# Optimization experiments

Measured on AMD Instinct MI355X. Metric: run time of the kernel, lower is better.

Reference implementation:

```python
import jax, jax.numpy as jnp
import numpy as np

N = 65536      # points
C = 256        # channels
K = 16         # knn_samples
L = 4          # num_blocks
EXP = 4        # MLP expansion
EPS = 1e-5


def layer_norm(x, g, b):
    m = jnp.mean(x, axis=-1, keepdims=True)
    v = jnp.var(x, axis=-1, keepdims=True)
    return (x - m) * jax.lax.rsqrt(v + EPS) * g + b


def setup_inputs() -> dict:
    key = jax.random.key(0)
    ks = jax.random.split(key, 16)
    s = lambda fan_in: 1.0 / np.sqrt(fan_in)
    inp = {
        "x": jax.random.normal(ks[0], (N, C), jnp.float32),
        "knn_idx": jax.random.randint(ks[1], (N, K), 0, N, jnp.int32),
        # per-block stacked params (PyTorch Linear stored as [in, out] here)
        "ln1_g": jnp.ones((L, C), jnp.float32),
        "ln1_b": jnp.zeros((L, C), jnp.float32),
        "w_qkv": jax.random.uniform(ks[2], (L, C, 3 * C), jnp.float32, -s(C), s(C)),
        "w_proj": jax.random.uniform(ks[3], (L, C, C), jnp.float32, -s(C), s(C)),
        "b_proj": jax.random.uniform(ks[4], (L, C), jnp.float32, -s(C), s(C)),
        "ln2_g": jnp.ones((L, C), jnp.float32),
        "ln2_b": jnp.zeros((L, C), jnp.float32),
        "w_fc1": jax.random.uniform(ks[5], (L, C, EXP * C), jnp.float32, -s(C), s(C)),
        "b_fc1": jax.random.uniform(ks[6], (L, EXP * C), jnp.float32, -s(C), s(C)),
        "w_fc2": jax.random.uniform(ks[7], (L, EXP * C, C), jnp.float32, -s(EXP * C), s(EXP * C)),
        "b_fc2": jax.random.uniform(ks[8], (L, C), jnp.float32, -s(EXP * C), s(EXP * C)),
    }
    return inp


def reference(x, knn_idx, ln1_g, ln1_b, w_qkv, w_proj, b_proj,
              ln2_g, ln2_b, w_fc1, b_fc1, w_fc2, b_fc2):
    scale = C ** (-0.5)  # head_dim == C (num_heads == 1)
    for i in range(L):
        # --- KNN attention ---
        h = layer_norm(x, ln1_g[i], ln1_b[i])
        qkv = h @ w_qkv[i]                       # [N, 3C], no bias
        q, k, v = jnp.split(qkv, 3, axis=-1)     # each [N, C]
        kk = k[knn_idx]                          # [N, K, C] neighbor gather
        vv = v[knn_idx]                          # [N, K, C]
        scores = jnp.einsum('nc,nkc->nk', q, kk) * scale
        attn = jax.nn.softmax(scores, axis=-1)   # softmax over K neighbors
        out = jnp.einsum('nk,nkc->nc', attn, vv)
        x = x + (out @ w_proj[i] + b_proj[i])
        # --- MLP ---
        h2 = layer_norm(x, ln2_g[i], ln2_b[i])
        h2 = jax.nn.gelu(h2 @ w_fc1[i] + b_fc1[i], approximate=False)
        x = x + (h2 @ w_fc2[i] + b_fc2[i])
    return x
```

## Files before the change

### kernel.cpp

```cpp
#include <hip/hip_runtime.h>

typedef __attribute__((ext_vector_type(4))) float  f32x4;
typedef __attribute__((ext_vector_type(2))) float  f32x2;
typedef __attribute__((ext_vector_type(8))) __bf16 bf16x8;
typedef __attribute__((ext_vector_type(4))) short  s16x4;
typedef __attribute__((ext_vector_type(8))) short  s16x8;
typedef unsigned char uchar;

__device__ __forceinline__ unsigned short f2bf(float f) {
  unsigned u = __builtin_bit_cast(unsigned, f);
  u += 0x7FFFu + ((u >> 16) & 1u);
  return (unsigned short)(u >> 16);
}
__device__ __forceinline__ float b2f(short s) {
  return __builtin_bit_cast(float, (unsigned)((unsigned short)s) << 16);
}
__device__ __forceinline__ uchar f2fp8(float v) {
  return (uchar)(__builtin_amdgcn_cvt_pk_fp8_f32(v, v, 0, false) & 0xFF);
}

__device__ __forceinline__ void gload16(const void* g, void* l) {
  __builtin_amdgcn_global_load_lds(
      (const __attribute__((address_space(1))) void*)g,
      (__attribute__((address_space(3))) void*)l, 16, 0, 0);
}

__global__ __launch_bounds__(256) void wcast(const float* __restrict__ W,
                                             short* __restrict__ WT,
                                             int In, int Out) {
  int i = blockIdx.x * 256 + threadIdx.x;
  int lay = blockIdx.y;
  if (i >= In * Out) return;
  const float* w = W + (size_t)lay * In * Out;
  short* wt = WT + (size_t)lay * In * Out;
  int ii = i % In, oo = i / In;
  wt[(size_t)oo * In + ii] = (short)f2bf(w[(size_t)ii * Out + oo]);
}

__global__ __launch_bounds__(256) void ln_k(const float* __restrict__ x,
                                            const float* __restrict__ g,
                                            const float* __restrict__ b,
                                            short* __restrict__ out) {
  int row = blockIdx.x * 4 + (threadIdx.x >> 6);
  int l = threadIdx.x & 63;
  const float4 v = *(const float4*)(x + (size_t)row * 256 + l * 4);
  float s  = v.x + v.y + v.z + v.w;
  float ss = v.x * v.x + v.y * v.y + v.z * v.z + v.w * v.w;
#pragma unroll
  for (int o = 32; o >= 1; o >>= 1) {
    s  += __shfl_xor(s, o);
    ss += __shfl_xor(ss, o);
  }
  float mean = s * (1.0f / 256.0f);
  float var  = ss * (1.0f / 256.0f) - mean * mean;
  float rstd = rsqrtf(var + 1e-5f);
  const float4 gg = *(const float4*)(g + l * 4);
  const float4 bb = *(const float4*)(b + l * 4);
  s16x4 o4;
  o4[0] = (short)f2bf((v.x - mean) * rstd * gg.x + bb.x);
  o4[1] = (short)f2bf((v.y - mean) * rstd * gg.y + bb.y);
  o4[2] = (short)f2bf((v.z - mean) * rstd * gg.z + bb.z);
  o4[3] = (short)f2bf((v.w - mean) * rstd * gg.w + bb.w);
  *(s16x4*)(out + (size_t)row * 256 + l * 4) = o4;
}

__global__ __launch_bounds__(256) void attn_k(const short* __restrict__ q_,
                                              const uchar* __restrict__ k8,
                                              const uchar* __restrict__ v8,
                                              const int* __restrict__ knn,
                                              short* __restrict__ out) {
  int n = blockIdx.x * 4 + (threadIdx.x >> 6);
  int l = threadIdx.x & 63;
  int j = l & 15, g = l >> 4;
  int idxj = knn[(size_t)n * 16 + j];
  const short* qp = q_ + (size_t)n * 256 + g * 64;
  const uchar* kp = k8 + (size_t)idxj * 256 + g * 64;
  float partial = 0.f;
#pragma unroll
  for (int t = 0; t < 4; ++t) {
    int4 kv = *(const int4*)(kp + t * 16);
    s16x8 q0 = *(const s16x8*)(qp + t * 16);
    s16x8 q1 = *(const s16x8*)(qp + t * 16 + 8);
    f32x2 a;
    a = __builtin_amdgcn_cvt_pk_f32_fp8(kv.x, false);
    partial += a[0] * b2f(q0[0]) + a[1] * b2f(q0[1]);
    a = __builtin_amdgcn_cvt_pk_f32_fp8(kv.x, true);
    partial += a[0] * b2f(q0[2]) + a[1] * b2f(q0[3]);
    a = __builtin_amdgcn_cvt_pk_f32_fp8(kv.y, false);
    partial += a[0] * b2f(q0[4]) + a[1] * b2f(q0[5]);
    a = __builtin_amdgcn_cvt_pk_f32_fp8(kv.y, true);
    partial += a[0] * b2f(q0[6]) + a[1] * b2f(q0[7]);
    a = __builtin_amdgcn_cvt_pk_f32_fp8(kv.z, false);
    partial += a[0] * b2f(q1[0]) + a[1] * b2f(q1[1]);
    a = __builtin_amdgcn_cvt_pk_f32_fp8(kv.z, true);
    partial += a[0] * b2f(q1[2]) + a[1] * b2f(q1[3]);
    a = __builtin_amdgcn_cvt_pk_f32_fp8(kv.w, false);
    partial += a[0] * b2f(q1[4]) + a[1] * b2f(q1[5]);
    a = __builtin_amdgcn_cvt_pk_f32_fp8(kv.w, true);
    partial += a[0] * b2f(q1[6]) + a[1] * b2f(q1[7]);
  }
  partial += __shfl_xor(partial, 16);
  partial += __shfl_xor(partial, 32);
  float score = partial * 0.0625f;
  float mx = score;
#pragma unroll
  for (int o = 1; o < 16; o <<= 1) mx = fmaxf(mx, __shfl_xor(mx, o));
  float e = __expf(score - mx);
  float sum = e;
#pragma unroll
  for (int o = 1; o < 16; o <<= 1) sum += __shfl_xor(sum, o);
  float attn = e / sum;
  float4 o4 = {0.f, 0.f, 0.f, 0.f};
#pragma unroll
  for (int jj = 0; jj < 16; ++jj) {
    float aj = __shfl(attn, jj);
    int   ij = __shfl(idxj, jj);
    int vv = *(const int*)(v8 + (size_t)ij * 256 + l * 4);
    f32x2 lo = __builtin_amdgcn_cvt_pk_f32_fp8(vv, false);
    f32x2 hi = __builtin_amdgcn_cvt_pk_f32_fp8(vv, true);
    o4.x += aj * lo[0];
    o4.y += aj * lo[1];
    o4.z += aj * hi[0];
    o4.w += aj * hi[1];
  }
  s16x4 ob;
  ob[0] = (short)f2bf(o4.x);
  ob[1] = (short)f2bf(o4.y);
  ob[2] = (short)f2bf(o4.z);
  ob[3] = (short)f2bf(o4.w);
  *(s16x4*)(out + (size_t)n * 256 + l * 4) = ob;
}

template <int EPI, int KD>
__global__ __launch_bounds__(256) void gemm_k(
    const short* __restrict__ A, const short* __restrict__ BT,
    const float* __restrict__ bias, const float* __restrict__ resid,
    short* __restrict__ outb, float* __restrict__ outf,
    uchar* __restrict__ k8, uchar* __restrict__ v8, int Nout, int gx) {
  __shared__ __align__(16) short lA[128 * 64];
  __shared__ __align__(16) short lB[128 * 64];
  const int tid = threadIdx.x;
  const int l = tid & 63, w = tid >> 6;
  const int nwg = gridDim.x;
  const int bid = blockIdx.x;
  const int swz = (bid & 7) * (nwg >> 3) + (bid >> 3);
  const int m0 = (swz / gx) << 7, n0 = (swz % gx) << 7;
  const int wm = w >> 1, wn = w & 1;

  f32x4 acc[4][4];
#pragma unroll
  for (int i = 0; i < 4; ++i)
#pragma unroll
    for (int jj = 0; jj < 4; ++jj) acc[i][jj] = f32x4{0.f, 0.f, 0.f, 0.f};

  const int srow = (w << 3) + (l >> 3);
  const int scol = (((l & 7) << 3)) ^ ((srow & 7) << 3);
  const short* gA = A + (size_t)(m0 + srow) * KD + scol;
  const short* gB = BT + (size_t)(n0 + srow) * KD + scol;

  for (int kt = 0; kt < KD; kt += 64) {
#pragma unroll
    for (int it = 0; it < 4; ++it) {
      gload16(gA + (size_t)(it * 32) * KD + kt, &lA[(it * 32 + w * 8) * 64]);
      gload16(gB + (size_t)(it * 32) * KD + kt, &lB[(it * 32 + w * 8) * 64]);
    }
    __syncthreads();
#pragma unroll
    for (int kc = 0; kc < 2; ++kc) {
      bf16x8 aF[4], bF[4];
#pragma unroll
      for (int f = 0; f < 4; ++f) {
        int r = wm * 64 + f * 16 + (l & 15);
        int ce = (kc * 32 + ((l >> 4) << 3)) ^ ((r & 7) << 3);
        aF[f] = *(const bf16x8*)(lA + r * 64 + ce);
      }
#pragma unroll
      for (int f = 0; f < 4; ++f) {
        int r = wn * 64 + f * 16 + (l & 15);
        int ce = (kc * 32 + ((l >> 4) << 3)) ^ ((r & 7) << 3);
        bF[f] = *(const bf16x8*)(lB + r * 64 + ce);
      }
#pragma unroll
      for (int mf = 0; mf < 4; ++mf)
#pragma unroll
        for (int nf = 0; nf < 4; ++nf)
          acc[mf][nf] = __builtin_amdgcn_mfma_f32_16x16x32_bf16(
              aF[mf], bF[nf], acc[mf][nf], 0, 0, 0);
    }
    __syncthreads();
  }

  const int lr = (l >> 4) << 2, lc = l & 15;
#pragma unroll
  for (int mf = 0; mf < 4; ++mf) {
#pragma unroll
    for (int nf = 0; nf < 4; ++nf) {
#pragma unroll
      for (int jj = 0; jj < 4; ++jj) {
        int row = m0 + wm * 64 + mf * 16 + lr + jj;
        int col = n0 + wn * 64 + nf * 16 + lc;
        float v = acc[mf][nf][jj];
        if (EPI == 1) {
          v += bias[col] + resid[(size_t)row * 256 + col];
          outf[(size_t)row * 256 + col] = v;
        } else if (EPI == 2) {
          v += bias[col];
          v = 0.5f * v * (1.f + erff(v * 0.70710678118654752440f));
          outb[(size_t)row * Nout + col] = (short)f2bf(v);
        } else {
          if (col < 256)
            outb[(size_t)row * 256 + col] = (short)f2bf(v);
          else if (col < 512)
            k8[(size_t)row * 256 + (col - 256)] = f2fp8(v);
          else
            v8[(size_t)row * 256 + (col - 512)] = f2fp8(v);
        }
      }
    }
  }
}

extern "C" void kernel_launch(void* const* d_in, const int* in_sizes, int n_in,
                              void* d_out, int out_size, void* d_ws, size_t ws_size,
                              hipStream_t stream) {
  const float* in_x   = (const float*)d_in[0];
  const int*   knn    = (const int*)d_in[1];
  const float* ln1_g  = (const float*)d_in[2];
  const float* ln1_b  = (const float*)d_in[3];
  const float* w_qkv  = (const float*)d_in[4];
  const float* w_proj = (const float*)d_in[5];
  const float* b_proj = (const float*)d_in[6];
  const float* ln2_g  = (const float*)d_in[7];
  const float* ln2_b  = (const float*)d_in[8];
  const float* w_fc1  = (const float*)d_in[9];
  const float* b_fc1  = (const float*)d_in[10];
  const float* w_fc2  = (const float*)d_in[11];
  const float* b_fc2  = (const float*)d_in[12];

  char* ws = (char*)d_ws;
  float* x   = (float*)(ws);
  short* act = (short*)(ws + 67108864);
  short* big = (short*)(ws + 100663296);
  short* q_bf = big;
  uchar* k8   = (uchar*)(ws + 100663296 + 33554432);
  uchar* v8   = (uchar*)(ws + 100663296 + 50331648);
  short* wT  = (short*)(ws + 234881024);
  short* wqkvT  = wT;
  short* wprojT = wT + 786432;
  short* wfc1T  = wT + 1048576;
  short* wfc2T  = wT + 2097152;

  wcast<<<dim3(768, 4), 256, 0, stream>>>(w_qkv, wqkvT, 256, 768);
  wcast<<<dim3(256, 4), 256, 0, stream>>>(w_proj, wprojT, 256, 256);
  wcast<<<dim3(1024, 4), 256, 0, stream>>>(w_fc1, wfc1T, 256, 1024);
  wcast<<<dim3(1024, 4), 256, 0, stream>>>(w_fc2, wfc2T, 1024, 256);

  for (int i = 0; i < 4; ++i) {
    const float* xin = (i == 0) ? in_x : x;
    ln_k<<<16384, 256, 0, stream>>>(xin, ln1_g + i * 256, ln1_b + i * 256, act);
    gemm_k<3, 256><<<3072, 256, 0, stream>>>(
        act, wqkvT + (size_t)i * 196608, nullptr, nullptr, q_bf, nullptr,
        k8, v8, 768, 6);
    attn_k<<<16384, 256, 0, stream>>>(q_bf, k8, v8, knn, act);
    gemm_k<1, 256><<<1024, 256, 0, stream>>>(
        act, wprojT + (size_t)i * 65536, b_proj + i * 256, xin, nullptr, x,
        nullptr, nullptr, 256, 2);
    ln_k<<<16384, 256, 0, stream>>>(x, ln2_g + i * 256, ln2_b + i * 256, act);
    gemm_k<2, 256><<<4096, 256, 0, stream>>>(
        act, wfc1T + (size_t)i * 262144, b_fc1 + i * 1024, nullptr, big, nullptr,
        nullptr, nullptr, 1024, 8);
    gemm_k<1, 1024><<<1024, 256, 0, stream>>>(
        big, wfc2T + (size_t)i * 262144, b_fc2 + i * 256, x, nullptr,
        (i == 3) ? (float*)d_out : x, nullptr, nullptr, 256, 2);
  }
}
```

Measured before the change: 1.320 ms.

## Fuse LayerNorm into residual GEMM epilogues and use tanh-approx GELU

Adds a gemm_ln kernel that computes a full 128x256 output row tile per workgroup. Its epilogue adds bias and residual, writes x, reduces row mean and variance across waves through LDS, and writes the next LayerNorm's bf16 activations. This removes the separate ln_k launches and their re-read of x, and prefetches LN1 for the next block. It also replaces erf-based GELU with a tanh approximation built on __expf. The wider tile raises register pressure (acc[4][8]), halves the grid to 512 workgroups, and the GELU approximation changes numerics.

```diff
diff --git a/kernel.cpp b/kernel.cpp
--- a/kernel.cpp
+++ b/kernel.cpp
@@ -17,6 +17,13 @@
 }
 __device__ __forceinline__ uchar f2fp8(float v) {
   return (uchar)(__builtin_amdgcn_cvt_pk_fp8_f32(v, v, 0, false) & 0xFF);
+}
+__device__ __forceinline__ float gelu_fast(float v) {
+  float u = v * (0.7978845608f + 0.0356774081f * v * v);
+  float t = __expf(-2.f * fabsf(u));
+  float th = (1.f - t) / (1.f + t);
+  th = (u >= 0.f) ? th : -th;
+  return 0.5f * v * (1.f + th);
 }
 
 __device__ __forceinline__ void gload16(const void* g, void* l) {
@@ -134,8 +141,7 @@
 template <int EPI, int KD>
 __global__ __launch_bounds__(256) void gemm_k(
     const short* __restrict__ A, const short* __restrict__ BT,
-    const float* __restrict__ bias, const float* __restrict__ resid,
-    short* __restrict__ outb, float* __restrict__ outf,
+    const float* __restrict__ bias, short* __restrict__ outb,
     uchar* __restrict__ k8, uchar* __restrict__ v8, int Nout, int gx) {
   __shared__ __align__(16) short lA[128 * 64];
   __shared__ __align__(16) short lB[128 * 64];
@@ -200,12 +206,8 @@
         int row = m0 + wm * 64 + mf * 16 + lr + jj;
         int col = n0 + wn * 64 + nf * 16 + lc;
         float v = acc[mf][nf][jj];
-        if (EPI == 1) {
-          v += bias[col] + resid[(size_t)row * 256 + col];
-          outf[(size_t)row * 256 + col] = v;
-        } else if (EPI == 2) {
-          v += bias[col];
-          v = 0.5f * v * (1.f + erff(v * 0.70710678118654752440f));
+        if (EPI == 2) {
+          v = gelu_fast(v + bias[col]);
           outb[(size_t)row * Nout + col] = (short)f2bf(v);
         } else {
           if (col < 256)
@@ -215,6 +217,117 @@
           else
             v8[(size_t)row * 256 + (col - 512)] = f2fp8(v);
         }
+      }
+    }
+  }
+}
+
+template <int KD>
+__global__ __launch_bounds__(256) void gemm_ln(
+    const short* __restrict__ A, const short* __restrict__ BT,
+    const float* __restrict__ bias, const float* __restrict__ resid,
+    float* __restrict__ xout, const float* __restrict__ lng,
+    const float* __restrict__ lnb, short* __restrict__ act) {
+  __shared__ __align__(16) short lA[128 * 64];
+  __shared__ __align__(16) short lB[256 * 64];
+  __shared__ float psum[2][128], psq[2][128];
+  const int tid = threadIdx.x;
+  const int l = tid & 63, w = tid >> 6;
+  const int nwg = gridDim.x;
+  const int bid = blockIdx.x;
+  const int swz = (bid & 7) * (nwg >> 3) + (bid >> 3);
+  const int m0 = swz << 7;
+  const int wm = w >> 1, wn = w & 1;
+
+  f32x4 acc[4][8];
+#pragma unroll
+  for (int i = 0; i < 4; ++i)
+#pragma unroll
+    for (int jj = 0; jj < 8; ++jj) acc[i][jj] = f32x4{0.f, 0.f, 0.f, 0.f};
+
+  const int srow = (w << 3) + (l >> 3);
+  const int scol = (((l & 7) << 3)) ^ ((srow & 7) << 3);
+  const short* gA = A + (size_t)(m0 + srow) * KD + scol;
+  const short* gB = BT + (size_t)srow * KD + scol;
+
+  for (int kt = 0; kt < KD; kt += 64) {
+#pragma unroll
+    for (int it = 0; it < 4; ++it)
+      gload16(gA + (size_t)(it * 32) * KD + kt, &lA[(it * 32 + w * 8) * 64]);
+#pragma unroll
+    for (int it = 0; it < 8; ++it)
+      gload16(gB + (size_t)(it * 32) * KD + kt, &lB[(it * 32 + w * 8) * 64]);
+    __syncthreads();
+#pragma unroll
+    for (int kc = 0; kc < 2; ++kc) {
+      bf16x8 aF[4], bF[8];
+#pragma unroll
+      for (int f = 0; f < 4; ++f) {
+        int r = wm * 64 + f * 16 + (l & 15);
+        int ce = (kc * 32 + ((l >> 4) << 3)) ^ ((r & 7) << 3);
+        aF[f] = *(const bf16x8*)(lA + r * 64 + ce);
+      }
+#pragma unroll
+      for (int f = 0; f < 8; ++f) {
+        int r = wn * 128 + f * 16 + (l & 15);
+        int ce = (kc * 32 + ((l >> 4) << 3)) ^ ((r & 7) << 3);
+        bF[f] = *(const bf16x8*)(lB + r * 64 + ce);
+      }
+#pragma unroll
+      for (int mf = 0; mf < 4; ++mf)
+#pragma unroll
+        for (int nf = 0; nf < 8; ++nf)
+          acc[mf][nf] = __builtin_amdgcn_mfma_f32_16x16x32_bf16(
+              aF[mf], bF[nf], acc[mf][nf], 0, 0, 0);
+    }
+    __syncthreads();
+  }
+
+  const int lr = (l >> 4) << 2, lc = l & 15;
+#pragma unroll
+  for (int mf = 0; mf < 4; ++mf) {
+#pragma unroll
+    for (int jj = 0; jj < 4; ++jj) {
+      int rowl = wm * 64 + mf * 16 + lr + jj;
+      int row = m0 + rowl;
+      float s = 0.f, q = 0.f;
+#pragma unroll
+      for (int nf = 0; nf < 8; ++nf) {
+        int col = wn * 128 + nf * 16 + lc;
+        float v = acc[mf][nf][jj] + bias[col] + resid[(size_t)row * 256 + col];
+        acc[mf][nf][jj] = v;
+        xout[(size_t)row * 256 + col] = v;
+        s += v;
+        q += v * v;
+      }
+#pragma unroll
+      for (int off = 1; off < 16; off <<= 1) {
+        s += __shfl_xor(s, off);
+        q += __shfl_xor(q, off);
+      }
+      if (lc == 0) {
+        psum[wn][rowl] = s;
+        psq[wn][rowl] = q;
+      }
+    }
+  }
+  __syncthreads();
+#pragma unroll
+  for (int mf = 0; mf < 4; ++mf) {
+#pragma unroll
+    for (int jj = 0; jj < 4; ++jj) {
+      int rowl = wm * 64 + mf * 16 + lr + jj;
+      int row = m0 + rowl;
+      float S = psum[0][rowl] + psum[1][rowl];
+      float Q = psq[0][rowl] + psq[1][rowl];
+      float mean = S * (1.0f / 256.0f);
+      float var = Q * (1.0f / 256.0f) - mean * mean;
+      float rstd = rsqrtf(var + 1e-5f);
+#pragma unroll
+      for (int nf = 0; nf < 8; ++nf) {
+        int col = wn * 128 + nf * 16 + lc;
+        float v = (acc[mf][nf][jj] - mean) * rstd * lng[col] + lnb[col];
+        act[(size_t)row * 256 + col] = (short)f2bf(v);
       }
     }
   }
@@ -238,13 +351,14 @@
   const float* b_fc2  = (const float*)d_in[12];
 
   char* ws = (char*)d_ws;
-  float* x   = (float*)(ws);
-  short* act = (short*)(ws + 67108864);
-  short* big = (short*)(ws + 100663296);
+  float* x    = (float*)(ws);
+  short* act  = (short*)(ws + 67108864);
+  short* big  = (short*)(ws + 100663296);
   short* q_bf = big;
-  uchar* k8   = (uchar*)(ws + 100663296 + 33554432);
-  uchar* v8   = (uchar*)(ws + 100663296 + 50331648);
-  short* wT  = (short*)(ws + 234881024);
+  uchar* k8   = (uchar*)(ws + 134217728);
+  uchar* v8   = (uchar*)(ws + 150994944);
+  short* attb = (short*)(ws + 167772160);
+  short* wT   = (short*)(ws + 234881024);
   short* wqkvT  = wT;
   short* wprojT = wT + 786432;
   short* wfc1T  = wT + 1048576;
@@ -255,22 +369,23 @@
   wcast<<<dim3(1024, 4), 256, 0, stream>>>(w_fc1, wfc1T, 256, 1024);
   wcast<<<dim3(1024, 4), 256, 0, stream>>>(w_fc2, wfc2T, 1024, 256);
 
+  ln_k<<<16384, 256, 0, stream>>>(in_x, ln1_g, ln1_b, act);
+
   for (int i = 0; i < 4; ++i) {
     const float* xin = (i == 0) ? in_x : x;
-    ln_k<<<16384, 256, 0, stream>>>(xin, ln1_g + i * 256, ln1_b + i * 256, act);
+    int inext = (i < 3) ? i + 1 : 3;
     gemm_k<3, 256><<<3072, 256, 0, stream>>>(
-        act, wqkvT + (size_t)i * 196608, nullptr, nullptr, q_bf, nullptr,
-        k8, v8, 768, 6);
-    attn_k<<<16384, 256, 0, stream>>>(q_bf, k8, v8, knn, act);
-    gemm_k<1, 256><<<1024, 256, 0, stream>>>(
-        act, wprojT + (size_t)i * 65536, b_proj + i * 256, xin, nullptr, x,
-        nullptr, nullptr, 256, 2);
-    ln_k<<<16384, 256, 0, stream>>>(x, ln2_g + i * 256, ln2_b + i * 256, act);
+        act, wqkvT + (size_t)i * 196608, nullptr, q_bf, k8, v8, 768, 6);
+    attn_k<<<16384, 256, 0, stream>>>(q_bf, k8, v8, knn, attb);
+    gemm_ln<256><<<512, 256, 0, stream>>>(
+        attb, wprojT + (size_t)i * 65536, b_proj + i * 256, xin, x,
+        ln2_g + i * 256, ln2_b + i * 256, act);
     gemm_k<2, 256><<<4096, 256, 0, stream>>>(
-        act, wfc1T + (size_t)i * 262144, b_fc1 + i * 1024, nullptr, big, nullptr,
+        act, wfc1T + (size_t)i * 262144, b_fc1 + i * 1024, big,
         nullptr, nullptr, 1024, 8);
-    gemm_k<1, 1024><<<1024, 256, 0, stream>>>(
-        big, wfc2T + (size_t)i * 262144, b_fc2 + i * 256, x, nullptr,
-        (i == 3) ? (float*)d_out : x, nullptr, nullptr, 256, 2);
-  }
-}
+    gemm_ln<1024><<<512, 256, 0, stream>>>(
+        big, wfc2T + (size_t)i * 262144, b_fc2 + i * 256, x,
+        (i == 3) ? (float*)d_out : x,
+        ln1_g + inext * 256, ln1_b + inext * 256, act);
+  }
+}
```

New measurement: 1.705 ms. 1.29x slower.
